# Optimization experiments

Hardware: AMD Instinct MI355X
Metric: run time of the kernel (lower is better)

The kernel has to match this reference:

```python
import jax, jax.numpy as jnp
import numpy as np

B, S, HID = 2, 2048, 2048
H, HKV, D = 16, 4, 128        # num_heads, num_kv_heads, head_dim
G = H // HKV                   # GQA group size
CLIP = 8.0                     # clip_qkv
THETA = 10000.0                # rope_theta_within_seq
N_SEQS = 8                     # max_num_sequences


def setup_inputs() -> dict:
    key = jax.random.key(0)
    ks = jax.random.split(key, 6)
    hidden_states = jax.random.normal(ks[0], (B, S, HID), dtype=jnp.float32)
    within_seq_position_ids = jnp.broadcast_to(jnp.arange(S, dtype=jnp.int64), (B, S))
    global_position_ids = jnp.broadcast_to(jnp.arange(S, dtype=jnp.int64), (B, S))
    sequence_ids = jnp.sort(jax.random.randint(ks[1], (B, S), 0, N_SEQS, dtype=jnp.int64), axis=-1)
    scale = 0.02
    Wq = jax.random.normal(ks[2], (H * D, HID), dtype=jnp.float32) * scale
    Wk = jax.random.normal(ks[3], (HKV * D, HID), dtype=jnp.float32) * scale
    Wv = jax.random.normal(ks[4], (HKV * D, HID), dtype=jnp.float32) * scale
    Wo = jax.random.normal(ks[5], (HID, H * D), dtype=jnp.float32) * scale
    return {"hidden_states": hidden_states,
            "within_seq_position_ids": within_seq_position_ids,
            "global_position_ids": global_position_ids,
            "sequence_ids": sequence_ids,
            "Wq": Wq, "Wk": Wk, "Wv": Wv, "Wo": Wo}


def _rotate_half(x):
    x1, x2 = jnp.split(x, 2, axis=-1)
    return jnp.concatenate((-x2, x1), axis=-1)


def _rope_cos_sin(position_ids, dtype):
    # inv_freq: [D/2]
    inv_freq = THETA ** (-(jnp.arange(0, D, 2, dtype=jnp.float32) / D))
    angles = position_ids.astype(jnp.float32)[..., None] * inv_freq  # [B,S,D/2]
    angles = jnp.concatenate((angles, angles), axis=-1)              # [B,S,D]
    # unsqueeze head dim -> [B,S,1,D]
    return jnp.cos(angles)[:, :, None, :].astype(dtype), jnp.sin(angles)[:, :, None, :].astype(dtype)


def reference(hidden_states, within_seq_position_ids, global_position_ids, sequence_ids, Wq, Wk, Wv, Wo):
    b, s, _ = hidden_states.shape
    q = (hidden_states @ Wq.T).reshape(b, s, H, D)
    k = (hidden_states @ Wk.T).reshape(b, s, HKV, D)
    v = (hidden_states @ Wv.T).reshape(b, s, HKV, D)
    # clip_qkv
    q = jnp.clip(q, -CLIP, CLIP)
    k = jnp.clip(k, -CLIP, CLIP)
    v = jnp.clip(v, -CLIP, CLIP)
    # RoPE (within_seq layer -> within_seq_position_ids)
    cos, sin = _rope_cos_sin(within_seq_position_ids, q.dtype)
    q = q * cos + _rotate_half(q) * sin
    k = k * cos + _rotate_half(k) * sin
    # GQA: group queries by kv head instead of materializing repeat_kv
    q = q.transpose(0, 2, 1, 3).reshape(b, HKV, G, s, D)  # [B,HKV,G,S,D]
    k = k.transpose(0, 2, 1, 3)                            # [B,HKV,S,D]
    v = v.transpose(0, 2, 1, 3)
    scores = jnp.einsum('bhgqd,bhkd->bhgqk', q, k) / jnp.sqrt(jnp.asarray(D, q.dtype))
    # block-diagonal (same sequence) causal mask
    qi = jnp.arange(s)
    causal = qi[:, None] >= qi[None, :]                    # [S,S]
    same_seq = sequence_ids[:, :, None] == sequence_ids[:, None, :]  # [B,S,S]
    mask = (causal[None] & same_seq)[:, None, None, :, :]  # [B,1,1,S,S]
    scores = jnp.where(mask, scores, jnp.finfo(scores.dtype).min)
    attn = jax.nn.softmax(scores, axis=-1)
    out = jnp.einsum('bhgqk,bhkd->bhgqd', attn, v)         # [B,HKV,G,S,D]
    out = out.reshape(b, H, s, D).transpose(0, 2, 1, 3).reshape(b, s, H * D)
    return out @ Wo.T
```

## Files before the change

### kernel.cpp

```cpp
#include <hip/hip_runtime.h>
#include <hip/hip_bf16.h>

typedef __hip_bfloat16 bf16;
typedef __attribute__((ext_vector_type(8))) short bf16x8;
typedef __attribute__((ext_vector_type(4))) float f32x4;

#define MFMA_BF16(a, b, c) __builtin_amdgcn_mfma_f32_16x16x32_bf16((a), (b), (c), 0, 0, 0)

#define B_   2
#define S_   2048
#define HID_ 2048
#define H_   16
#define HKV_ 4
#define D_   128

#define GLOAD_LDS(gptr, lptr) \
  __builtin_amdgcn_global_load_lds((const __attribute__((address_space(1))) void*)(gptr), \
                                   (__attribute__((address_space(3))) void*)(lptr), 16, 0, 0)

template <int N>
__device__ __forceinline__ void vmw() {
  if constexpr (N == 0)      asm volatile("s_waitcnt vmcnt(0)" ::: "memory");
  else if constexpr (N == 2) asm volatile("s_waitcnt vmcnt(2)" ::: "memory");
  else if constexpr (N == 3) asm volatile("s_waitcnt vmcnt(3)" ::: "memory");
  else if constexpr (N == 4) asm volatile("s_waitcnt vmcnt(4)" ::: "memory");
  else if constexpr (N == 5) asm volatile("s_waitcnt vmcnt(5)" ::: "memory");
  else                       asm volatile("s_waitcnt vmcnt(6)" ::: "memory");
}

__device__ __forceinline__ void blk_barrier() {
  __builtin_amdgcn_sched_barrier(0);
  __builtin_amdgcn_s_barrier();
  __builtin_amdgcn_sched_barrier(0);
}

__global__ void cvt_f32_bf16(const float* __restrict__ src, bf16* __restrict__ dst, int n) {
  int i = (blockIdx.x * 256 + threadIdx.x) * 4;
  if (i >= n) return;
  float4 v = *reinterpret_cast<const float4*>(src + i);
  alignas(8) bf16 t[4];
  t[0] = __float2bfloat16(v.x);
  t[1] = __float2bfloat16(v.y);
  t[2] = __float2bfloat16(v.z);
  t[3] = __float2bfloat16(v.w);
  *reinterpret_cast<short4*>(dst + i) = *reinterpret_cast<const short4*>(t);
}

__global__ void cvt_weights(const float* __restrict__ Wq, const float* __restrict__ Wk,
                            const float* __restrict__ Wv, const float* __restrict__ Wo,
                            bf16* __restrict__ Wqkv, bf16* __restrict__ Wob) {
  int i = (blockIdx.x * 256 + threadIdx.x) * 4;
  const float* src; bf16* dst; int off;
  if (i < 4194304)      { src = Wq; dst = Wqkv;           off = i; }
  else if (i < 5242880) { src = Wk; dst = Wqkv + 4194304; off = i - 4194304; }
  else if (i < 6291456) { src = Wv; dst = Wqkv + 5242880; off = i - 5242880; }
  else                  { src = Wo; dst = Wob;            off = i - 6291456; }
  float4 v = *reinterpret_cast<const float4*>(src + off);
  alignas(8) bf16 t[4];
  t[0] = __float2bfloat16(v.x);
  t[1] = __float2bfloat16(v.y);
  t[2] = __float2bfloat16(v.z);
  t[3] = __float2bfloat16(v.w);
  *reinterpret_cast<short4*>(dst + off) = *reinterpret_cast<const short4*>(t);
}

__global__ void seq_start(const int* __restrict__ seq, int* __restrict__ sstart) {
  int t = blockIdx.x * 256 + threadIdx.x;
  int b = t >> 11, s = t & (S_ - 1);
  const int* sb = seq + b * S_;
  int sid = sb[s];
  int lo = 0, hi = s;
  while (lo < hi) {
    int mid = (lo + hi) >> 1;
    if (sb[mid] < sid) lo = mid + 1; else hi = mid;
  }
  sstart[t] = lo;
}

template <int BM, int BN, int OUT_BF16>
__global__ __launch_bounds__(512, 2) void gemm8p(const bf16* __restrict__ A,
                                                 const bf16* __restrict__ Bw,
                                                 void* __restrict__ Cout,
                                                 int M, int N, int K) {
  constexpr int MR = BM / 32;
  constexpr int NR = BN / 64;
  constexpr int LA = BM / 128;

  __shared__ bf16 As[2][2][BM * 32];
  __shared__ bf16 Bs[2][2][BN * 32];

  const int tid  = threadIdx.x;
  const int lane = tid & 63;
  const int w    = tid >> 6;
  const int wr   = w >> 2;
  const int wc   = w & 3;
  const int ln15 = lane & 15, g = lane >> 4;

  const int nwg = gridDim.x;
  int bid = blockIdx.x;
  bid = (bid & 7) * (nwg >> 3) + (bid >> 3);
  const int nbn = N / BN;
  const int m0 = (bid / nbn) * BM;
  const int n0 = (bid % nbn) * BN;

  f32x4 acc[MR][NR] = {};

  auto stageA = [&](int db, int kh, int t) {
    int kc = t * 64 + kh * 32;
#pragma unroll
    for (int r = 0; r < LA; r++) {
      int sIdx = r * 512 + tid;
      int row = sIdx >> 2;
      int ss = (sIdx & 3) ^ ((row >> 1) & 3);
      GLOAD_LDS(A + (size_t)(m0 + row) * K + kc + ss * 8, &As[db][kh][(r * 512 + w * 64) * 8]);
    }
  };
  auto stageB_r = [&](int db, int t, int r) {
    int slot = r * 512 + tid;
    int frow = slot >> 2;
    int kh = frow >= BN;
    int brow = frow - kh * BN;
    int ss = (slot & 3) ^ ((brow >> 1) & 3);
    GLOAD_LDS(Bw + (size_t)(n0 + brow) * K + t * 64 + kh * 32 + ss * 8,
              &Bs[db][0][0] + (size_t)(r * 512 + w * 64) * 8);
  };
  auto stageB_h = [&](int db, int kh, int t) {
    int brow = tid >> 2;
    int ss = (tid & 3) ^ ((brow >> 1) & 3);
    GLOAD_LDS(Bw + (size_t)(n0 + brow) * K + t * 64 + kh * 32 + ss * 8,
              &Bs[db][kh][(w * 64) * 8]);
  };

  bf16x8 af[4], bfr[NR];
  auto rdA = [&](int db, int kh, int mb) {
#pragma unroll
    for (int m = 0; m < 4; m++) {
      int row = wr * (BM / 2) + (mb + m) * 16 + ln15;
      af[m] = *reinterpret_cast<const bf16x8*>(&As[db][kh][row * 32 + ((g ^ ((row >> 1) & 3)) << 3)]);
    }
  };
  auto rdB = [&](int db, int kh) {
#pragma unroll
    for (int n = 0; n < NR; n++) {
      int row = wc * (BN / 4) + n * 16 + ln15;
      bfr[n] = *reinterpret_cast<const bf16x8*>(&Bs[db][kh][row * 32 + ((g ^ ((row >> 1) & 3)) << 3)]);
    }
  };
  auto MF = [&](int mb) {
    __builtin_amdgcn_s_setprio(1);
#pragma unroll
    for (int m = 0; m < 4; m++)
#pragma unroll
      for (int n = 0; n < NR; n++)
        acc[mb + m][n] = MFMA_BF16(af[m], bfr[n], acc[mb + m][n]);
    __builtin_amdgcn_s_setprio(0);
  };

  const int NT = K >> 6;

  if constexpr (BN == 192) {
    stageA(0, 0, 0);
    stageB_r(0, 0, 0); stageB_r(0, 0, 1);
    stageA(0, 1, 0);
    stageB_r(0, 0, 2);
    stageA(1, 0, 1);
    vmw<5>();
  } else {
    stageA(0, 0, 0);
    stageB_h(0, 0, 0);
    stageA(0, 1, 0);
    stageB_h(0, 1, 0);
    stageA(1, 0, 1);
    stageB_h(1, 0, 1);
    vmw<6>();
  }
  blk_barrier();

  for (int T = 0; T < NT; ++T) {
    const int db = T & 1, dn = db ^ 1;
    const bool tail = (T >= NT - 2);

    rdA(db, 0, 0); rdB(db, 0);
    if (T + 1 < NT) stageA(dn, 1, T + 1);
    blk_barrier(); MF(0); blk_barrier();
    rdA(db, 0, 4);
    if constexpr (BN == 192) {
      if (T + 1 < NT) { stageB_r(dn, T + 1, 0); stageB_r(dn, T + 1, 1); }
      if (tail) vmw<0>(); else vmw<4>();
    } else {
      if (T + 1 < NT) stageB_h(dn, 1, T + 1);
      if (tail) vmw<0>(); else vmw<6>();
    }
    blk_barrier(); MF(4); blk_barrier();
    rdA(db, 1, 0); rdB(db, 1);
    if (T + 2 < NT) stageA(db, 0, T + 2);
    blk_barrier(); MF(0); blk_barrier();
    rdA(db, 1, 4);
    if constexpr (BN == 192) {
      if (T + 1 < NT) stageB_r(dn, T + 1, 2);
      if (tail) vmw<0>(); else vmw<3>();
    } else {
      if (T + 2 < NT) stageB_h(db, 0, T + 2);
      if (tail) vmw<0>(); else vmw<6>();
    }
    blk_barrier(); MF(4); blk_barrier();
  }

#pragma unroll
  for (int m = 0; m < MR; m++)
#pragma unroll
    for (int n = 0; n < NR; n++)
#pragma unroll
      for (int r = 0; r < 4; r++) {
        int row = m0 + wr * (BM / 2) + m * 16 + g * 4 + r;
        int col = n0 + wc * (BN / 4) + n * 16 + ln15;
        if constexpr (OUT_BF16) {
          ((bf16*)Cout)[(size_t)row * N + col] = __float2bfloat16(acc[m][n][r]);
        } else {
          ((float*)Cout)[(size_t)row * N + col] = acc[m][n][r];
        }
      }
}

__global__ __launch_bounds__(256) void qkv_post(const bf16* __restrict__ QKV,
                                                const int* __restrict__ wpos,
                                                bf16* __restrict__ Qs,
                                                bf16* __restrict__ Ks,
                                                bf16* __restrict__ Vt) {
  const int row = blockIdx.x;
  const int b = row >> 11, s = row & (S_ - 1);
  const int t = threadIdx.x;
  const bf16* R = QKV + (size_t)row * 3072;
  const float pos = (float)wpos[row];
  const float kln = 0.14391156831212787f;
  const float qscale = 0.08838834764831845f;

  for (int p = t; p < 1024; p += 256) {
    int h = p >> 6, i = p & 63;
    float ang = pos * expf(-(float)i * kln);
    float sn, cs;
    sincosf(ang, &sn, &cs);
    float x1 = __bfloat162float(R[h * 128 + i]);
    float x2 = __bfloat162float(R[h * 128 + 64 + i]);
    x1 = fminf(fmaxf(x1, -8.f), 8.f);
    x2 = fminf(fmaxf(x2, -8.f), 8.f);
    float y1 = (x1 * cs - x2 * sn) * qscale;
    float y2 = (x2 * cs + x1 * sn) * qscale;
    size_t qb = ((size_t)(b * H_ + h) * S_ + s) * D_;
    Qs[qb + i]      = __float2bfloat16(y1);
    Qs[qb + 64 + i] = __float2bfloat16(y2);
  }
  {
    int kh = t >> 6, i = t & 63;
    float ang = pos * expf(-(float)i * kln);
    float sn, cs;
    sincosf(ang, &sn, &cs);
    float x1 = __bfloat162float(R[2048 + kh * 128 + i]);
    float x2 = __bfloat162float(R[2048 + kh * 128 + 64 + i]);
    x1 = fminf(fmaxf(x1, -8.f), 8.f);
    x2 = fminf(fmaxf(x2, -8.f), 8.f);
    float y1 = x1 * cs - x2 * sn;
    float y2 = x2 * cs + x1 * sn;
    size_t kb = ((size_t)(b * HKV_ + kh) * S_ + s) * D_;
    Ks[kb + i]      = __float2bfloat16(y1);
    Ks[kb + 64 + i] = __float2bfloat16(y2);
  }
  for (int e = t; e < 512; e += 256) {
    int kh = e >> 7, d = e & 127;
    float x = __bfloat162float(R[2560 + e]);
    x = fminf(fmaxf(x, -8.f), 8.f);
    Vt[((size_t)(b * HKV_ + kh) * D_ + d) * S_ + s] = __float2bfloat16(x);
  }
}

__global__ __launch_bounds__(256) void attn_fwd(const bf16* __restrict__ Qs,
                                                const bf16* __restrict__ Ks,
                                                const bf16* __restrict__ Vt,
                                                const int* __restrict__ sstart,
                                                bf16* __restrict__ att) {
  __shared__ bf16 Kl[2][32 * 128];
  __shared__ bf16 Vl[2][128 * 32];
  __shared__ bf16 Plds[4][16 * 32];

  const int tid = threadIdx.x;
  const int lane = tid & 63, w = tid >> 6;
  const int ln15 = lane & 15, g = lane >> 4;

  const int wg = ((blockIdx.x & 7) << 7) | (blockIdx.x >> 3);
  const int qt  = wg & 127;
  const int kvh = (wg >> 7) & 3;
  const int b   = wg >> 9;
  const int h   = kvh * 4 + w;
  const int q0  = qt * 16;
  const int qi  = q0 + ln15;

  const bf16* Qrow = Qs + ((size_t)(b * H_ + h) * S_ + qi) * D_;
  bf16x8 qf[4];
#pragma unroll
  for (int c = 0; c < 4; c++)
    qf[c] = *reinterpret_cast<const bf16x8*>(Qrow + c * 32 + g * 8);

  const int sQ = sstart[b * S_ + qi];
  const int kstart = __builtin_amdgcn_readfirstlane(__shfl(sQ, 0));
  const int kend = q0 + 15;

  const bf16* Kb = Ks + (size_t)(b * HKV_ + kvh) * S_ * D_;
  const bf16* Vb = Vt + (size_t)(b * HKV_ + kvh) * D_ * S_;

  auto stage = [&](int buf, int kb) {
#pragma unroll
    for (int p = 0; p < 2; p++) {
      int slot = p * 256 + tid;
      int row = slot >> 4;
      int cs = (slot & 15) ^ (row & 15);
      int gr = min(kb + row, S_ - 1);
      GLOAD_LDS(Kb + (size_t)gr * D_ + cs * 8, &Kl[buf][(p * 256 + w * 64) * 8]);
    }
#pragma unroll
    for (int p = 0; p < 2; p++) {
      int slot = p * 256 + tid;
      int d = slot >> 2, c = slot & 3;
      int cs = c ^ (d & 3);
      int gcol = min(kb + cs * 8, S_ - 8);
      GLOAD_LDS(Vb + (size_t)d * S_ + gcol, &Vl[buf][(p * 256 + w * 64) * 8]);
    }
  };

  float m = -1e30f, lsum = 0.f;
  f32x4 o[8] = {};

  stage(0, kstart);
  int buf = 0;
  for (int kb = kstart; kb <= kend; kb += 32) {
    __syncthreads();
    if (kb + 32 <= kend) stage(buf ^ 1, kb + 32);

    bf16x8 kf0[4], kf1[4];
#pragma unroll
    for (int c = 0; c < 4; c++) {
      kf0[c] = *reinterpret_cast<const bf16x8*>(&Kl[buf][ln15 * 128 + (((c * 4 + g) ^ ln15) << 3)]);
      kf1[c] = *reinterpret_cast<const bf16x8*>(&Kl[buf][(16 + ln15) * 128 + (((c * 4 + g) ^ ln15) << 3)]);
    }
    f32x4 s0 = {0.f, 0.f, 0.f, 0.f}, s1 = {0.f, 0.f, 0.f, 0.f};
#pragma unroll
    for (int c = 0; c < 4; c++) {
      s0 = MFMA_BF16(kf0[c], qf[c], s0);
      s1 = MFMA_BF16(kf1[c], qf[c], s1);
    }

    float sc[8];
    float tmax = -1e30f;
#pragma unroll
    for (int r = 0; r < 4; r++) {
      int k0i = kb + g * 4 + r;
      int k1i = k0i + 16;
      float x0 = (k0i >= sQ && k0i <= qi) ? s0[r] : -1e30f;
      float x1 = (k1i >= sQ && k1i <= qi) ? s1[r] : -1e30f;
      sc[r] = x0;
      sc[4 + r] = x1;
      tmax = fmaxf(tmax, fmaxf(x0, x1));
    }
    tmax = fmaxf(tmax, __shfl_xor(tmax, 16));
    tmax = fmaxf(tmax, __shfl_xor(tmax, 32));
    float mn  = fmaxf(m, tmax);
    float fac = __expf(m - mn);
    float ps = 0.f;
    alignas(16) bf16 pb[8];
#pragma unroll
    for (int i2 = 0; i2 < 8; i2++) {
      float p = (sc[i2] < -1e29f) ? 0.f : __expf(sc[i2] - mn);
      ps += p;
      pb[i2] = __float2bfloat16(p);
    }
    ps += __shfl_xor(ps, 16);
    ps += __shfl_xor(ps, 32);
    lsum = lsum * fac + ps;
    m = mn;
#pragma unroll
    for (int t2 = 0; t2 < 8; t2++) o[t2] *= fac;

    *reinterpret_cast<short4*>(&Plds[w][ln15 * 32 + g * 4])      = *reinterpret_cast<const short4*>(&pb[0]);
    *reinterpret_cast<short4*>(&Plds[w][ln15 * 32 + 16 + g * 4]) = *reinterpret_cast<const short4*>(&pb[4]);
    __builtin_amdgcn_wave_barrier();
    bf16x8 pf = *reinterpret_cast<const bf16x8*>(&Plds[w][ln15 * 32 + g * 8]);

#pragma unroll
    for (int t2 = 0; t2 < 8; t2++) {
      int d = t2 * 16 + ln15;
      bf16x8 vf = *reinterpret_cast<const bf16x8*>(&Vl[buf][d * 32 + ((g ^ (ln15 & 3)) << 3)]);
      o[t2] = MFMA_BF16(vf, pf, o[t2]);
    }
    __builtin_amdgcn_wave_barrier();
    buf ^= 1;
  }

  float inv = 1.f / lsum;
#pragma unroll
  for (int t2 = 0; t2 < 8; t2++)
#pragma unroll
    for (int r = 0; r < 4; r++) {
      int d = t2 * 16 + g * 4 + r;
      att[((size_t)(b * S_ + qi)) * (H_ * D_) + h * D_ + d] = __float2bfloat16(o[t2][r] * inv);
    }
}

extern "C" void kernel_launch(void* const* d_in, const int* in_sizes, int n_in,
                              void* d_out, int out_size, void* d_ws, size_t ws_size,
                              hipStream_t stream) {
  const float* hidden = (const float*)d_in[0];
  const int* wpos = (const int*)d_in[1];
  const int* seq = (const int*)d_in[3];
  const float* Wq = (const float*)d_in[4];
  const float* Wk = (const float*)d_in[5];
  const float* Wv = (const float*)d_in[6];
  const float* Wo = (const float*)d_in[7];

  char* ws = (char*)d_ws;
  bf16* Xb   = (bf16*)(ws);
  bf16* Wqkv = (bf16*)(ws + 16777216);
  bf16* Wob  = (bf16*)(ws + 29360128);
  bf16* QKVb = (bf16*)(ws + 37748736);
  bf16* Ksb  = (bf16*)(ws + 62914560);
  bf16* Vtb  = (bf16*)(ws + 67108864);
  int*  sst  = (int*)(ws + 71303168);
  bf16* Qsb  = Xb;
  bf16* attb = QKVb;

  cvt_f32_bf16<<<dim3(8192), dim3(256), 0, stream>>>(hidden, Xb, 8388608);
  cvt_weights<<<dim3(10240), dim3(256), 0, stream>>>(Wq, Wk, Wv, Wo, Wqkv, Wob);
  seq_start<<<dim3(32), dim3(256), 0, stream>>>(seq, sst);

  gemm8p<256, 192, 1><<<dim3(256), dim3(512), 0, stream>>>(Xb, Wqkv, (void*)QKVb, 4096, 3072, 2048);

  qkv_post<<<dim3(4096), dim3(256), 0, stream>>>(QKVb, wpos, Qsb, Ksb, Vtb);

  attn_fwd<<<dim3(1024), dim3(256), 0, stream>>>(Qsb, Ksb, Vtb, sst, attb);

  gemm8p<256, 128, 0><<<dim3(256), dim3(512), 0, stream>>>(attb, Wob, d_out, 4096, 2048, 2048);
}
```

Measured before the change: 179.2 us.

## Restage GEMM B tiles as full 64-wide K blocks and merge conversion kernels

Merges the hidden-state and weight fp32→bf16 conversion kernels into a single launch. In the GEMM, the B operand is now staged as one full 64-wide K tile per buffer with an 8-way XOR swizzle, loaded two tiles ahead, with a single unified vmcnt wait per iteration in place of the separate per-BN staging paths. This is meant to cut launch overhead and simplify and deepen B prefetch. In exchange, LDS use for B changes and the wait counts must match the new load ordering, which risks stalls or hazards if the count is off.

```diff
diff --git a/kernel.cpp b/kernel.cpp
--- a/kernel.cpp
+++ b/kernel.cpp
@@ -21,8 +21,6 @@
 template <int N>
 __device__ __forceinline__ void vmw() {
   if constexpr (N == 0)      asm volatile("s_waitcnt vmcnt(0)" ::: "memory");
-  else if constexpr (N == 2) asm volatile("s_waitcnt vmcnt(2)" ::: "memory");
-  else if constexpr (N == 3) asm volatile("s_waitcnt vmcnt(3)" ::: "memory");
   else if constexpr (N == 4) asm volatile("s_waitcnt vmcnt(4)" ::: "memory");
   else if constexpr (N == 5) asm volatile("s_waitcnt vmcnt(5)" ::: "memory");
   else                       asm volatile("s_waitcnt vmcnt(6)" ::: "memory");
@@ -34,34 +32,24 @@
   __builtin_amdgcn_sched_barrier(0);
 }
 
-__global__ void cvt_f32_bf16(const float* __restrict__ src, bf16* __restrict__ dst, int n) {
-  int i = (blockIdx.x * 256 + threadIdx.x) * 4;
-  if (i >= n) return;
-  float4 v = *reinterpret_cast<const float4*>(src + i);
+__global__ void cvt_all(const float* __restrict__ hidden, const float* __restrict__ Wq,
+                        const float* __restrict__ Wk, const float* __restrict__ Wv,
+                        const float* __restrict__ Wo,
+                        bf16* __restrict__ Xb, bf16* __restrict__ Wqkv, bf16* __restrict__ Wob) {
+  long long i4 = (long long)blockIdx.x * 256 + threadIdx.x;
+  const float* src; bf16* dst; long long off;
+  if (i4 < 2097152)      { src = hidden; dst = Xb;             off = i4; }
+  else if (i4 < 3145728) { src = Wq;     dst = Wqkv;           off = i4 - 2097152; }
+  else if (i4 < 3407872) { src = Wk;     dst = Wqkv + 4194304; off = i4 - 3145728; }
+  else if (i4 < 3670016) { src = Wv;     dst = Wqkv + 5242880; off = i4 - 3407872; }
+  else                   { src = Wo;     dst = Wob;            off = i4 - 3670016; }
+  float4 v = *reinterpret_cast<const float4*>(src + off * 4);
   alignas(8) bf16 t[4];
   t[0] = __float2bfloat16(v.x);
   t[1] = __float2bfloat16(v.y);
   t[2] = __float2bfloat16(v.z);
   t[3] = __float2bfloat16(v.w);
-  *reinterpret_cast<short4*>(dst + i) = *reinterpret_cast<const short4*>(t);
-}
-
-__global__ void cvt_weights(const float* __restrict__ Wq, const float* __restrict__ Wk,
-                            const float* __restrict__ Wv, const float* __restrict__ Wo,
-                            bf16* __restrict__ Wqkv, bf16* __restrict__ Wob) {
-  int i = (blockIdx.x * 256 + threadIdx.x) * 4;
-  const float* src; bf16* dst; int off;
-  if (i < 4194304)      { src = Wq; dst = Wqkv;           off = i; }
-  else if (i < 5242880) { src = Wk; dst = Wqkv + 4194304; off = i - 4194304; }
-  else if (i < 6291456) { src = Wv; dst = Wqkv + 5242880; off = i - 5242880; }
-  else                  { src = Wo; dst = Wob;            off = i - 6291456; }
-  float4 v = *reinterpret_cast<const float4*>(src + off);
-  alignas(8) bf16 t[4];
-  t[0] = __float2bfloat16(v.x);
-  t[1] = __float2bfloat16(v.y);
-  t[2] = __float2bfloat16(v.z);
-  t[3] = __float2bfloat16(v.w);
-  *reinterpret_cast<short4*>(dst + off) = *reinterpret_cast<const short4*>(t);
+  *reinterpret_cast<short4*>(dst + off * 4) = *reinterpret_cast<const short4*>(t);
 }
 
 __global__ void seq_start(const int* __restrict__ seq, int* __restrict__ sstart) {
@@ -85,9 +73,10 @@
   constexpr int MR = BM / 32;
   constexpr int NR = BN / 64;
   constexpr int LA = BM / 128;
+  constexpr int QD = NR + 2;
 
   __shared__ bf16 As[2][2][BM * 32];
-  __shared__ bf16 Bs[2][2][BN * 32];
+  __shared__ bf16 Bs[2][BN * 64];
 
   const int tid  = threadIdx.x;
   const int lane = tid & 63;
@@ -115,20 +104,14 @@
       GLOAD_LDS(A + (size_t)(m0 + row) * K + kc + ss * 8, &As[db][kh][(r * 512 + w * 64) * 8]);
     }
   };
-  auto stageB_r = [&](int db, int t, int r) {
-    int slot = r * 512 + tid;
-    int frow = slot >> 2;
-    int kh = frow >= BN;
-    int brow = frow - kh * BN;
-    int ss = (slot & 3) ^ ((brow >> 1) & 3);
-    GLOAD_LDS(Bw + (size_t)(n0 + brow) * K + t * 64 + kh * 32 + ss * 8,
-              &Bs[db][0][0] + (size_t)(r * 512 + w * 64) * 8);
-  };
-  auto stageB_h = [&](int db, int kh, int t) {
-    int brow = tid >> 2;
-    int ss = (tid & 3) ^ ((brow >> 1) & 3);
-    GLOAD_LDS(Bw + (size_t)(n0 + brow) * K + t * 64 + kh * 32 + ss * 8,
-              &Bs[db][kh][(w * 64) * 8]);
+  auto stageB = [&](int db, int t) {
+#pragma unroll
+    for (int r = 0; r < NR; r++) {
+      int sIdx = r * 512 + tid;
+      int row = sIdx >> 3;
+      int cs = (sIdx & 7) ^ (row & 7);
+      GLOAD_LDS(Bw + (size_t)(n0 + row) * K + t * 64 + cs * 8, &Bs[db][(size_t)(r * 512 + w * 64) * 8]);
+    }
   };
 
   bf16x8 af[4], bfr[NR];
@@ -143,7 +126,8 @@
 #pragma unroll
     for (int n = 0; n < NR; n++) {
       int row = wc * (BN / 4) + n * 16 + ln15;
-      bfr[n] = *reinterpret_cast<const bf16x8*>(&Bs[db][kh][row * 32 + ((g ^ ((row >> 1) & 3)) << 3)]);
+      int sl = ((kh << 2) + g) ^ (row & 7);
+      bfr[n] = *reinterpret_cast<const bf16x8*>(&Bs[db][row * 64 + sl * 8]);
     }
   };
   auto MF = [&](int mb) {
@@ -158,50 +142,29 @@
 
   const int NT = K >> 6;
 
-  if constexpr (BN == 192) {
-    stageA(0, 0, 0);
-    stageB_r(0, 0, 0); stageB_r(0, 0, 1);
-    stageA(0, 1, 0);
-    stageB_r(0, 0, 2);
-    stageA(1, 0, 1);
-    vmw<5>();
-  } else {
-    stageA(0, 0, 0);
-    stageB_h(0, 0, 0);
-    stageA(0, 1, 0);
-    stageB_h(0, 1, 0);
-    stageA(1, 0, 1);
-    stageB_h(1, 0, 1);
-    vmw<6>();
-  }
+  stageA(0, 0, 0);
+  stageA(0, 1, 0);
+  stageB(0, 0);
+  stageA(1, 0, 1);
+  stageB(1, 1);
+  vmw<QD>();
   blk_barrier();
 
   for (int T = 0; T < NT; ++T) {
     const int db = T & 1, dn = db ^ 1;
-    const bool tail = (T >= NT - 2);
 
     rdA(db, 0, 0); rdB(db, 0);
     if (T + 1 < NT) stageA(dn, 1, T + 1);
     blk_barrier(); MF(0); blk_barrier();
     rdA(db, 0, 4);
-    if constexpr (BN == 192) {
-      if (T + 1 < NT) { stageB_r(dn, T + 1, 0); stageB_r(dn, T + 1, 1); }
-      if (tail) vmw<0>(); else vmw<4>();
-    } else {
-      if (T + 1 < NT) stageB_h(dn, 1, T + 1);
-      if (tail) vmw<0>(); else vmw<6>();
-    }
     blk_barrier(); MF(4); blk_barrier();
     rdA(db, 1, 0); rdB(db, 1);
     if (T + 2 < NT) stageA(db, 0, T + 2);
     blk_barrier(); MF(0); blk_barrier();
     rdA(db, 1, 4);
-    if constexpr (BN == 192) {
-      if (T + 1 < NT) stageB_r(dn, T + 1, 2);
-      if (tail) vmw<0>(); else vmw<3>();
-    } else {
-      if (T + 2 < NT) stageB_h(db, 0, T + 2);
-      if (tail) vmw<0>(); else vmw<6>();
+    if (T + 2 < NT) stageB(db, T + 2);
+    if (T + 1 < NT) {
+      if (T == NT - 2) vmw<0>(); else vmw<QD>();
     }
     blk_barrier(); MF(4); blk_barrier();
   }
@@ -426,8 +389,7 @@
   bf16* Qsb  = Xb;
   bf16* attb = QKVb;
 
-  cvt_f32_bf16<<<dim3(8192), dim3(256), 0, stream>>>(hidden, Xb, 8388608);
-  cvt_weights<<<dim3(10240), dim3(256), 0, stream>>>(Wq, Wk, Wv, Wo, Wqkv, Wob);
+  cvt_all<<<dim3(18432), dim3(256), 0, stream>>>(hidden, Wq, Wk, Wv, Wo, Xb, Wqkv, Wob);
   seq_start<<<dim3(32), dim3(256), 0, stream>>>(seq, sst);
 
   gemm8p<256, 192, 1><<<dim3(256), dim3(512), 0, stream>>>(Xb, Wqkv, (void*)QKVb, 4096, 3072, 2048);
```

After: 174.7 us. 2.5% less time.
